# Kernel tuning notes

Hardware: AMD Instinct MI355X
Metric: run time of the kernel (lower is better)

Reference implementation:

```python
import jax, jax.numpy as jnp
import numpy as np

# --- PGA G(3,0,1) algebra tables, blade order matches gatr/ezgatr convention ---
_BLADES = [(), (0,), (1,), (2,), (3,), (0, 1), (0, 2), (0, 3), (1, 2), (1, 3), (2, 3),
           (0, 1, 2), (0, 1, 3), (0, 2, 3), (1, 2, 3), (0, 1, 2, 3)]
_IDX = {b: i for i, b in enumerate(_BLADES)}
_METRIC = (0, 1, 1, 1)  # e0^2 = 0, e1^2 = e2^2 = e3^2 = 1


def _mul_blades(a, b):
    elems = list(a) + list(b)
    sign = 1
    done = False
    while not done:
        done = True
        t = 0
        while t < len(elems) - 1:
            if elems[t] == elems[t + 1]:
                if _METRIC[elems[t]] == 0:
                    return 0, ()
                del elems[t + 1], elems[t]
                done = False
            elif elems[t] > elems[t + 1]:
                elems[t], elems[t + 1] = elems[t + 1], elems[t]
                sign = -sign
                done = False
                t += 1
            else:
                t += 1
    return sign, tuple(elems)


def _perm_sign(seq):
    inv = sum(1 for i in range(len(seq)) for j in range(i + 1, len(seq)) if seq[i] > seq[j])
    return -1 if inv % 2 else 1


def _build_tables():
    # geometric product Cayley table: x*y = einsum('ijk,i,j->k', GP, x, y)
    gp = np.zeros((16, 16, 16), np.float32)
    for i, a in enumerate(_BLADES):
        for j, b in enumerate(_BLADES):
            s, r = _mul_blades(a, b)
            if s:
                gp[i, j, _IDX[r]] = s
    # right-complement dual: dual(e_b) = dsign[b] * e_comp(b), with e_b ^ dual(e_b) = e0123
    comp = {b: tuple(e for e in range(4) if e not in b) for b in _BLADES}
    dsign = {b: _perm_sign(list(b) + list(comp[b])) for b in _BLADES}
    # join Cayley table: J(x, y) = undual(dual(x) ^ dual(y))
    jc = np.zeros((16, 16, 16), np.float32)
    for i, a in enumerate(_BLADES):
        for j, b in enumerate(_BLADES):
            da, db = comp[a], comp[b]
            if set(da) & set(db):
                continue
            w = _perm_sign(list(da) + list(db))  # wedge sign
            m = tuple(sorted(da + db))
            k = comp[m]  # undual(e_m) = dsign[k] * e_k since dual(e_k) = dsign[k] * e_m
            jc[i, j, _IDX[k]] = dsign[a] * dsign[b] * w * dsign[k]
    # EquiLinear basis: 5 grade projections + 4 maps 'left-multiply by e0'; [9, out16, in16]
    basis = np.zeros((9, 16, 16), np.float32)
    for idx, b in enumerate(_BLADES):
        basis[len(b), idx, idx] = 1.0
        if 0 not in b and len(b) < 4:
            basis[5 + len(b), _IDX[(0,) + b], idx] = 1.0  # e0 * e_b = +e_{0b}
    return gp, jc, basis


_GP, _JC, _BASIS = _build_tables()
GP = jnp.asarray(_GP)
JC = jnp.asarray(_JC)
BASIS = jnp.asarray(_BASIS)


def equi_linear(x, w, b):
    # x: [..., c_in, 16], w: [c_out, c_in, 9], b: [c_out] bias on scalar component
    out = jnp.einsum('oia,akj,...ij->...ok', w, BASIS, x)
    return out.at[..., 0].add(b)


def setup_inputs() -> dict:
    key = jax.random.key(0)
    ks = jax.random.split(key, 6)
    B, T, H, I = 8, 8192, 32, 32  # batch, context, hidden channels, intermediate channels
    x = jax.random.normal(ks[0], (B, T, H, 16), jnp.float32)
    ref = jax.random.normal(ks[1], (B, T, 1, 16), jnp.float32)
    w_bil = jax.random.normal(ks[2], (2 * I, H, 9), jnp.float32) / np.sqrt(9.0 * H)
    b_bil = jax.random.normal(ks[3], (2 * I,), jnp.float32) * 0.02
    w_out = jax.random.normal(ks[4], (H, I, 9), jnp.float32) / np.sqrt(9.0 * I)
    b_out = jax.random.normal(ks[5], (H,), jnp.float32) * 0.02
    return {"x": x, "ref": ref, "w_bil": w_bil, "b_bil": b_bil, "w_out": w_out, "b_out": b_out}


def reference(x, ref, w_bil, b_bil, w_out, b_out):
    h = equi_linear(x, w_bil, b_bil)  # [B, T, 2*I, 16]
    si = h.shape[-2] // 4             # size_channels_intermediate // 2
    lg, rg, lj, rj = (h[..., t * si:(t + 1) * si, :] for t in range(4))
    gp = jnp.einsum('ijk,...ci,...cj->...ck', GP, lg, rg)
    join = ref[..., 15:16] * jnp.einsum('ijk,...ci,...cj->...ck', JC, lj, rj)
    return equi_linear(jnp.concatenate([gp, join], axis=-2), w_out, b_out)
```

## Files before the change

kernel.cpp:

```cpp
#include <hip/hip_runtime.h>

typedef unsigned int uint_t;

constexpr int MASK_OF_IDX[16] = {0,1,2,4,8,3,5,9,6,10,12,7,11,13,14,15};
constexpr int IDX_OF_MASK[16] = {0,1,2,5,3,6,8,11,4,7,9,12,10,13,14,15};

constexpr int popc4(int v){ int c=0; for(int b=0;b<4;++b) c += (v>>b)&1; return c; }
constexpr int reorder_sign(int a,int b){ int s=0; for(int j=0;j<4;++j) if((b>>j)&1) s += popc4(a>>(j+1)); return (s&1)?-1:1; }
constexpr int dsign_mask(int m){ int comp=(~m)&15; int s=0; for(int j=0;j<4;++j) if((comp>>j)&1) s += popc4(m>>(j+1)); return (s&1)?-1:1; }

struct Tab { int n; int e[256]; };
constexpr Tab build_gp(){
  Tab t{}; t.n=0;
  for(int i=0;i<16;++i) for(int j=0;j<16;++j){
    int a=MASK_OF_IDX[i], b=MASK_OF_IDX[j];
    if(a&b&1) continue;
    int k=IDX_OF_MASK[a^b];
    int s=reorder_sign(a,b);
    t.e[t.n++] = i | (j<<4) | (k<<8) | ((s<0)?(1<<12):0);
  }
  return t;
}
constexpr Tab build_jc(){
  Tab t{}; t.n=0;
  for(int i=0;i<16;++i) for(int j=0;j<16;++j){
    int a=MASK_OF_IDX[i], b=MASK_OF_IDX[j];
    int da=(~a)&15, db=(~b)&15;
    if(da&db) continue;
    int m=da|db, km=(~m)&15;
    int k=IDX_OF_MASK[km];
    int s=reorder_sign(da,db)*dsign_mask(a)*dsign_mask(b)*dsign_mask(km);
    t.e[t.n++] = i | (j<<4) | (k<<8) | ((s<0)?(1<<12):0);
  }
  return t;
}
constexpr Tab GPT = build_gp();
constexpr Tab JCT = build_jc();
static_assert(GPT.n==192, "gp nnz");
static_assert(JCT.n==81,  "jc nnz");

__device__ __forceinline__ void eqstepv(float* acc, const float* xv, const float4* w4){
  float w[12];
  *reinterpret_cast<float4*>(w+0) = w4[0];
  *reinterpret_cast<float4*>(w+4) = w4[1];
  *reinterpret_cast<float4*>(w+8) = w4[2];
  constexpr int G[16] = {0,1,1,1,1,2,2,2,2,2,2,3,3,3,3,4};
#pragma unroll
  for (int k=0;k<16;++k) acc[k] += w[G[k]]*xv[k];
  acc[1]  += w[5]*xv[0];
  acc[5]  += w[6]*xv[2];
  acc[6]  += w[6]*xv[3];
  acc[7]  += w[6]*xv[4];
  acc[11] += w[7]*xv[8];
  acc[12] += w[7]*xv[9];
  acc[13] += w[7]*xv[10];
  acc[15] += w[8]*xv[14];
}

#define TT   64
#define NTHR 1024
#define WP1_FLOATS (32*16*48)
#define WP3_FLOATS (32*16*24)

__global__ void gatr_pack_w(const float* __restrict__ wbil,
                            const float* __restrict__ wout,
                            float* __restrict__ wp){
  int tid = blockIdx.x*blockDim.x + threadIdx.x;
  if (tid < WP1_FLOATS){
    int k = tid % 12, q = (tid/12)&3, c = (tid/48)&15, i = tid/768;
    wp[tid] = (k<9) ? wbil[(((q<<4)+c)*32 + i)*9 + k] : 0.f;
  } else if (tid < WP1_FLOATS + WP3_FLOATS){
    int u = tid - WP1_FLOATS;
    int k = u % 12, h = (u/12)&1, g = (u/24)&15, ci = u/384;
    wp[tid] = (k<9) ? wout[(((h<<4)+g)*32 + ci)*9 + k] : 0.f;
  }
}

__global__ __launch_bounds__(NTHR, 4) void gatr_fused_kernel(
    const float* __restrict__ xg, const float* __restrict__ refg,
    const float* __restrict__ wp, const float* __restrict__ bbilg,
    const float* __restrict__ boutg, float* __restrict__ outg)
{
  __shared__ float4 LB[TT * 128];

  const int tid = threadIdx.x;
  const size_t tok0 = (size_t)blockIdx.x * TT;
  const int t = tid & 63;
  const int c = __builtin_amdgcn_readfirstlane(tid >> 6);

  const float refv = refg[(tok0 + t)*16 + 15];

  {
    const float4* xg4 = reinterpret_cast<const float4*>(xg + tok0*512);
#pragma unroll
    for (int j=0;j<8;++j){
      int g = tid + j*NTHR;
      int tau = g >> 7, f4 = g & 127;
      LB[(tau<<7) + ((f4 + tau) & 127)] = xg4[g];
    }
  }
  __syncthreads();

  const int tbase = t << 7;

  float gp[16], jn[16];
  {
    float A0[16], A1[16], A2[16], A3[16];
#pragma unroll
    for (int k=0;k<16;++k){ A0[k]=0.f; A1[k]=0.f; A2[k]=0.f; A3[k]=0.f; }

    const float4* w4 = reinterpret_cast<const float4*>(wp) + c*12;
    for (int i=0;i<32;++i){
      float xv[16];
      const int o = (i<<2) + t;
      *reinterpret_cast<float4*>(xv+ 0) = LB[tbase + ( o      & 127)];
      *reinterpret_cast<float4*>(xv+ 4) = LB[tbase + ((o + 1) & 127)];
      *reinterpret_cast<float4*>(xv+ 8) = LB[tbase + ((o + 2) & 127)];
      *reinterpret_cast<float4*>(xv+12) = LB[tbase + ((o + 3) & 127)];
      eqstepv(A0, xv, w4 + 0);
      eqstepv(A1, xv, w4 + 3);
      eqstepv(A2, xv, w4 + 6);
      eqstepv(A3, xv, w4 + 9);
      w4 += 192;
    }
    A0[0] += bbilg[c];
    A1[0] += bbilg[c + 16];
    A2[0] += bbilg[c + 32];
    A3[0] += bbilg[c + 48];

#pragma unroll
    for (int k=0;k<16;++k){ gp[k]=0.f; jn[k]=0.f; }
#pragma unroll
    for (int e=0;e<192;++e){
      const int p = GPT.e[e];
      float v = A0[p & 15] * A1[(p >> 4) & 15];
      if (p & (1<<12)) gp[(p >> 8) & 15] -= v; else gp[(p >> 8) & 15] += v;
    }
#pragma unroll
    for (int e=0;e<81;++e){
      const int p = JCT.e[e];
      float v = A2[p & 15] * A3[(p >> 4) & 15];
      if (p & (1<<12)) jn[(p >> 8) & 15] -= v; else jn[(p >> 8) & 15] += v;
    }
#pragma unroll
    for (int k=0;k<16;++k) jn[k] *= refv;
  }
  __syncthreads();

  {
#pragma unroll
    for (int r=0;r<4;++r){
      LB[tbase + (((c     )*4 + r + t) & 127)] = make_float4(gp[4*r], gp[4*r+1], gp[4*r+2], gp[4*r+3]);
      LB[tbase + (((c + 16)*4 + r + t) & 127)] = make_float4(jn[4*r], jn[4*r+1], jn[4*r+2], jn[4*r+3]);
    }
  }
  __syncthreads();

  float B0a[16], B1a[16];
  {
#pragma unroll
    for (int k=0;k<16;++k){ B0a[k]=0.f; B1a[k]=0.f; }

    const float4* w6 = reinterpret_cast<const float4*>(wp + WP1_FLOATS) + c*6;
    for (int cin=0; cin<32; ++cin){
      float yv[16];
      const int o = (cin<<2) + t;
      *reinterpret_cast<float4*>(yv+ 0) = LB[tbase + ( o      & 127)];
      *reinterpret_cast<float4*>(yv+ 4) = LB[tbase + ((o + 1) & 127)];
      *reinterpret_cast<float4*>(yv+ 8) = LB[tbase + ((o + 2) & 127)];
      *reinterpret_cast<float4*>(yv+12) = LB[tbase + ((o + 3) & 127)];
      eqstepv(B0a, yv, w6 + 0);
      eqstepv(B1a, yv, w6 + 3);
      w6 += 96;
    }
    B0a[0] += boutg[c];
    B1a[0] += boutg[c + 16];
  }
  __syncthreads();

  {
#pragma unroll
    for (int r=0;r<4;++r){
      LB[tbase + (((c     )*4 + r + t) & 127)] = make_float4(B0a[4*r], B0a[4*r+1], B0a[4*r+2], B0a[4*r+3]);
      LB[tbase + (((c + 16)*4 + r + t) & 127)] = make_float4(B1a[4*r], B1a[4*r+1], B1a[4*r+2], B1a[4*r+3]);
    }
  }
  __syncthreads();
  {
    float4* og4 = reinterpret_cast<float4*>(outg + tok0*512);
#pragma unroll
    for (int j=0;j<8;++j){
      int g = tid + j*NTHR;
      int tau = g >> 7, f4 = g & 127;
      og4[g] = LB[(tau<<7) + ((f4 + tau) & 127)];
    }
  }
}

extern "C" void kernel_launch(void* const* d_in, const int* in_sizes, int n_in,
                              void* d_out, int out_size, void* d_ws, size_t ws_size,
                              hipStream_t stream) {
  const float* x    = (const float*)d_in[0];
  const float* ref  = (const float*)d_in[1];
  const float* wbil = (const float*)d_in[2];
  const float* bbil = (const float*)d_in[3];
  const float* wout = (const float*)d_in[4];
  const float* bout = (const float*)d_in[5];
  float* out = (float*)d_out;
  float* wp  = (float*)d_ws;

  hipLaunchKernelGGL(gatr_pack_w,
                     dim3((WP1_FLOATS + WP3_FLOATS + 255)/256), dim3(256), 0, stream,
                     wbil, wout, wp);

  const int ntok = in_sizes[0] / 512;
  const int grid = ntok / TT;
  hipLaunchKernelGGL(gatr_fused_kernel, dim3(grid), dim3(NTHR), 0, stream,
                     x, ref, wp, bbil, bout, out);
}
```

Measured before the change: 427.9 us.

## Halve LDS tile by staging channels in two passes and store output directly

The shared buffer shrinks from 128 to 64 float4 per token. The input is loaded in two halves of 16 channels, and the gp and join results are staged one after the other through the same smaller buffer, so more blocks can fit per CU (launch bounds raised to 8). The final transposed write-out through LDS is replaced by direct per-thread float4 stores of each output row. This adds extra barriers and leaves the global stores uncoalesced, since each thread writes 64 bytes at a 2KB token stride. The tighter register budget from the higher occupancy target also risks spills.

New measurement: 1.645 ms. 285% more time.

```diff
diff --git a/kernel.cpp b/kernel.cpp
--- a/kernel.cpp
+++ b/kernel.cpp
@@ -38,6 +38,14 @@
 constexpr Tab JCT = build_jc();
 static_assert(GPT.n==192, "gp nnz");
 static_assert(JCT.n==81,  "jc nnz");
+
+__device__ __forceinline__ void st16(float* p, const float* v){
+  float4* q = (float4*)p;
+  q[0] = make_float4(v[0],v[1],v[2],v[3]);
+  q[1] = make_float4(v[4],v[5],v[6],v[7]);
+  q[2] = make_float4(v[8],v[9],v[10],v[11]);
+  q[3] = make_float4(v[12],v[13],v[14],v[15]);
+}
 
 __device__ __forceinline__ void eqstepv(float* acc, const float* xv, const float4* w4){
   float w[12];
@@ -76,12 +84,12 @@
   }
 }
 
-__global__ __launch_bounds__(NTHR, 4) void gatr_fused_kernel(
+__global__ __launch_bounds__(NTHR, 8) void gatr_fused_kernel(
     const float* __restrict__ xg, const float* __restrict__ refg,
     const float* __restrict__ wp, const float* __restrict__ bbilg,
     const float* __restrict__ boutg, float* __restrict__ outg)
 {
-  __shared__ float4 LB[TT * 128];
+  __shared__ float4 LB[TT * 64];
 
   const int tid = threadIdx.x;
   const size_t tok0 = (size_t)blockIdx.x * TT;
@@ -90,111 +98,112 @@
 
   const float refv = refg[(tok0 + t)*16 + 15];
 
-  {
-    const float4* xg4 = reinterpret_cast<const float4*>(xg + tok0*512);
-#pragma unroll
-    for (int j=0;j<8;++j){
+  const int tbase = t << 6;
+
+  float A0[16], A1[16], A2[16], A3[16];
+#pragma unroll
+  for (int k=0;k<16;++k){ A0[k]=0.f; A1[k]=0.f; A2[k]=0.f; A3[k]=0.f; }
+
+  const float4* w4 = reinterpret_cast<const float4*>(wp) + c*12;
+  const float4* xg4 = reinterpret_cast<const float4*>(xg + tok0*512);
+
+  for (int h=0; h<2; ++h){
+#pragma unroll
+    for (int j=0;j<4;++j){
       int g = tid + j*NTHR;
-      int tau = g >> 7, f4 = g & 127;
-      LB[(tau<<7) + ((f4 + tau) & 127)] = xg4[g];
+      int tau = g >> 6, s = g & 63;
+      LB[(tau<<6) + ((s + tau) & 63)] = xg4[tau*128 + h*64 + s];
     }
-  }
-  __syncthreads();
-
-  const int tbase = t << 7;
-
-  float gp[16], jn[16];
-  {
-    float A0[16], A1[16], A2[16], A3[16];
-#pragma unroll
-    for (int k=0;k<16;++k){ A0[k]=0.f; A1[k]=0.f; A2[k]=0.f; A3[k]=0.f; }
-
-    const float4* w4 = reinterpret_cast<const float4*>(wp) + c*12;
-    for (int i=0;i<32;++i){
+    __syncthreads();
+
+    for (int ii=0; ii<16; ++ii){
       float xv[16];
-      const int o = (i<<2) + t;
-      *reinterpret_cast<float4*>(xv+ 0) = LB[tbase + ( o      & 127)];
-      *reinterpret_cast<float4*>(xv+ 4) = LB[tbase + ((o + 1) & 127)];
-      *reinterpret_cast<float4*>(xv+ 8) = LB[tbase + ((o + 2) & 127)];
-      *reinterpret_cast<float4*>(xv+12) = LB[tbase + ((o + 3) & 127)];
+      const int o = (ii<<2) + t;
+      *reinterpret_cast<float4*>(xv+ 0) = LB[tbase + ( o      & 63)];
+      *reinterpret_cast<float4*>(xv+ 4) = LB[tbase + ((o + 1) & 63)];
+      *reinterpret_cast<float4*>(xv+ 8) = LB[tbase + ((o + 2) & 63)];
+      *reinterpret_cast<float4*>(xv+12) = LB[tbase + ((o + 3) & 63)];
       eqstepv(A0, xv, w4 + 0);
       eqstepv(A1, xv, w4 + 3);
       eqstepv(A2, xv, w4 + 6);
       eqstepv(A3, xv, w4 + 9);
       w4 += 192;
     }
-    A0[0] += bbilg[c];
-    A1[0] += bbilg[c + 16];
-    A2[0] += bbilg[c + 32];
-    A3[0] += bbilg[c + 48];
-
-#pragma unroll
-    for (int k=0;k<16;++k){ gp[k]=0.f; jn[k]=0.f; }
-#pragma unroll
-    for (int e=0;e<192;++e){
-      const int p = GPT.e[e];
-      float v = A0[p & 15] * A1[(p >> 4) & 15];
-      if (p & (1<<12)) gp[(p >> 8) & 15] -= v; else gp[(p >> 8) & 15] += v;
-    }
-#pragma unroll
-    for (int e=0;e<81;++e){
-      const int p = JCT.e[e];
-      float v = A2[p & 15] * A3[(p >> 4) & 15];
-      if (p & (1<<12)) jn[(p >> 8) & 15] -= v; else jn[(p >> 8) & 15] += v;
-    }
-#pragma unroll
-    for (int k=0;k<16;++k) jn[k] *= refv;
-  }
+    __syncthreads();
+  }
+
+  A0[0] += bbilg[c];
+  A1[0] += bbilg[c + 16];
+  A2[0] += bbilg[c + 32];
+  A3[0] += bbilg[c + 48];
+
+  float gp[16];
+#pragma unroll
+  for (int k=0;k<16;++k) gp[k]=0.f;
+#pragma unroll
+  for (int e=0;e<192;++e){
+    const int p = GPT.e[e];
+    float v = A0[p & 15] * A1[(p >> 4) & 15];
+    if (p & (1<<12)) gp[(p >> 8) & 15] -= v; else gp[(p >> 8) & 15] += v;
+  }
+#pragma unroll
+  for (int r=0;r<4;++r)
+    LB[tbase + (((c<<2) + r + t) & 63)] = make_float4(gp[4*r], gp[4*r+1], gp[4*r+2], gp[4*r+3]);
+
+  float jn[16];
+#pragma unroll
+  for (int k=0;k<16;++k) jn[k]=0.f;
+#pragma unroll
+  for (int e=0;e<81;++e){
+    const int p = JCT.e[e];
+    float v = A2[p & 15] * A3[(p >> 4) & 15];
+    if (p & (1<<12)) jn[(p >> 8) & 15] -= v; else jn[(p >> 8) & 15] += v;
+  }
+#pragma unroll
+  for (int k=0;k<16;++k) jn[k] *= refv;
+
   __syncthreads();
 
-  {
-#pragma unroll
-    for (int r=0;r<4;++r){
-      LB[tbase + (((c     )*4 + r + t) & 127)] = make_float4(gp[4*r], gp[4*r+1], gp[4*r+2], gp[4*r+3]);
-      LB[tbase + (((c + 16)*4 + r + t) & 127)] = make_float4(jn[4*r], jn[4*r+1], jn[4*r+2], jn[4*r+3]);
-    }
+  float B0a[16], B1a[16];
+#pragma unroll
+  for (int k=0;k<16;++k){ B0a[k]=0.f; B1a[k]=0.f; }
+
+  const float4* w6 = reinterpret_cast<const float4*>(wp + WP1_FLOATS) + c*6;
+  for (int cin=0; cin<16; ++cin){
+    float yv[16];
+    const int o = (cin<<2) + t;
+    *reinterpret_cast<float4*>(yv+ 0) = LB[tbase + ( o      & 63)];
+    *reinterpret_cast<float4*>(yv+ 4) = LB[tbase + ((o + 1) & 63)];
+    *reinterpret_cast<float4*>(yv+ 8) = LB[tbase + ((o + 2) & 63)];
+    *reinterpret_cast<float4*>(yv+12) = LB[tbase + ((o + 3) & 63)];
+    eqstepv(B0a, yv, w6 + 0);
+    eqstepv(B1a, yv, w6 + 3);
+    w6 += 96;
   }
   __syncthreads();
 
-  float B0a[16], B1a[16];
-  {
-#pragma unroll
-    for (int k=0;k<16;++k){ B0a[k]=0.f; B1a[k]=0.f; }
-
-    const float4* w6 = reinterpret_cast<const float4*>(wp + WP1_FLOATS) + c*6;
-    for (int cin=0; cin<32; ++cin){
-      float yv[16];
-      const int o = (cin<<2) + t;
-      *reinterpret_cast<float4*>(yv+ 0) = LB[tbase + ( o      & 127)];
-      *reinterpret_cast<float4*>(yv+ 4) = LB[tbase + ((o + 1) & 127)];
-      *reinterpret_cast<float4*>(yv+ 8) = LB[tbase + ((o + 2) & 127)];
-      *reinterpret_cast<float4*>(yv+12) = LB[tbase + ((o + 3) & 127)];
-      eqstepv(B0a, yv, w6 + 0);
-      eqstepv(B1a, yv, w6 + 3);
-      w6 += 96;
-    }
-    B0a[0] += boutg[c];
-    B1a[0] += boutg[c + 16];
-  }
+#pragma unroll
+  for (int r=0;r<4;++r)
+    LB[tbase + (((c<<2) + r + t) & 63)] = make_float4(jn[4*r], jn[4*r+1], jn[4*r+2], jn[4*r+3]);
   __syncthreads();
 
-  {
-#pragma unroll
-    for (int r=0;r<4;++r){
-      LB[tbase + (((c     )*4 + r + t) & 127)] = make_float4(B0a[4*r], B0a[4*r+1], B0a[4*r+2], B0a[4*r+3]);
-      LB[tbase + (((c + 16)*4 + r + t) & 127)] = make_float4(B1a[4*r], B1a[4*r+1], B1a[4*r+2], B1a[4*r+3]);
-    }
-  }
-  __syncthreads();
-  {
-    float4* og4 = reinterpret_cast<float4*>(outg + tok0*512);
-#pragma unroll
-    for (int j=0;j<8;++j){
-      int g = tid + j*NTHR;
-      int tau = g >> 7, f4 = g & 127;
-      og4[g] = LB[(tau<<7) + ((f4 + tau) & 127)];
-    }
-  }
+  for (int cin=0; cin<16; ++cin){
+    float yv[16];
+    const int o = (cin<<2) + t;
+    *reinterpret_cast<float4*>(yv+ 0) = LB[tbase + ( o      & 63)];
+    *reinterpret_cast<float4*>(yv+ 4) = LB[tbase + ((o + 1) & 63)];
+    *reinterpret_cast<float4*>(yv+ 8) = LB[tbase + ((o + 2) & 63)];
+    *reinterpret_cast<float4*>(yv+12) = LB[tbase + ((o + 3) & 63)];
+    eqstepv(B0a, yv, w6 + 0);
+    eqstepv(B1a, yv, w6 + 3);
+    w6 += 96;
+  }
+  B0a[0] += boutg[c];
+  B1a[0] += boutg[c + 16];
+
+  float* orow = outg + (tok0 + t)*512;
+  st16(orow + (c     )*16, B0a);
+  st16(orow + (c + 16)*16, B1a);
 }
 
 extern "C" void kernel_launch(void* const* d_in, const int* in_sizes, int n_in,
```

## Split fused GATr kernel into two kernels with global intermediate buffer

Applied to the files above, without the earlier changes.

Splits the single fused kernel into two: the first computes the bilinear layer and the geometric/join products and writes the intermediate to a channel-major global workspace, and the second reads it back and applies the output equi-linear layer. This removes two block-wide barriers and the shared-memory round trips between stages, and each kernel may get lower register pressure. In exchange it adds a full write and read of a 128 MB intermediate through global memory plus an extra launch. The old fused kernel is kept as a fallback when the workspace is too small.

Result: slower. 478.0 us (+11.7%).

```diff
diff --git a/kernel.cpp b/kernel.cpp
--- a/kernel.cpp
+++ b/kernel.cpp
@@ -39,6 +39,14 @@
 static_assert(GPT.n==192, "gp nnz");
 static_assert(JCT.n==81,  "jc nnz");
 
+__device__ __forceinline__ void st16(float* p, const float* v){
+  float4* q = (float4*)p;
+  q[0] = make_float4(v[0],v[1],v[2],v[3]);
+  q[1] = make_float4(v[4],v[5],v[6],v[7]);
+  q[2] = make_float4(v[8],v[9],v[10],v[11]);
+  q[3] = make_float4(v[12],v[13],v[14],v[15]);
+}
+
 __device__ __forceinline__ void eqstepv(float* acc, const float* xv, const float4* w4){
   float w[12];
   *reinterpret_cast<float4*>(w+0) = w4[0];
@@ -61,6 +69,7 @@
 #define NTHR 1024
 #define WP1_FLOATS (32*16*48)
 #define WP3_FLOATS (32*16*24)
+#define WP_FLOATS  (WP1_FLOATS + WP3_FLOATS)
 
 __global__ void gatr_pack_w(const float* __restrict__ wbil,
                             const float* __restrict__ wout,
@@ -74,6 +83,134 @@
     int k = u % 12, h = (u/12)&1, g = (u/24)&15, ci = u/384;
     wp[tid] = (k<9) ? wout[(((h<<4)+g)*32 + ci)*9 + k] : 0.f;
   }
+}
+
+
+__global__ __launch_bounds__(NTHR, 4) void gatr_p12(
+    const float* __restrict__ xg, const float* __restrict__ refg,
+    const float* __restrict__ wp, const float* __restrict__ bbilg,
+    float4* __restrict__ yt, int ntok)
+{
+  __shared__ float4 LB[TT * 128];
+
+  const int tid = threadIdx.x;
+  const size_t tok0 = (size_t)blockIdx.x * TT;
+  const int t = tid & 63;
+  const int c = __builtin_amdgcn_readfirstlane(tid >> 6);
+
+  const float refv = refg[(tok0 + t)*16 + 15];
+
+  {
+    const float4* xg4 = reinterpret_cast<const float4*>(xg + tok0*512);
+#pragma unroll
+    for (int j=0;j<8;++j){
+      int g = tid + j*NTHR;
+      int tau = g >> 7, f4 = g & 127;
+      LB[(tau<<7) + ((f4 + tau) & 127)] = xg4[g];
+    }
+  }
+  __syncthreads();
+
+  const int tbase = t << 7;
+
+  float A0[16], A1[16], A2[16], A3[16];
+#pragma unroll
+  for (int k=0;k<16;++k){ A0[k]=0.f; A1[k]=0.f; A2[k]=0.f; A3[k]=0.f; }
+
+  const float4* w4 = reinterpret_cast<const float4*>(wp) + c*12;
+  for (int i=0;i<32;++i){
+    float xv[16];
+    const int o = (i<<2) + t;
+    *reinterpret_cast<float4*>(xv+ 0) = LB[tbase + ( o      & 127)];
+    *reinterpret_cast<float4*>(xv+ 4) = LB[tbase + ((o + 1) & 127)];
+    *reinterpret_cast<float4*>(xv+ 8) = LB[tbase + ((o + 2) & 127)];
+    *reinterpret_cast<float4*>(xv+12) = LB[tbase + ((o + 3) & 127)];
+    eqstepv(A0, xv, w4 + 0);
+    eqstepv(A1, xv, w4 + 3);
+    eqstepv(A2, xv, w4 + 6);
+    eqstepv(A3, xv, w4 + 9);
+    w4 += 192;
+  }
+  A0[0] += bbilg[c];
+  A1[0] += bbilg[c + 16];
+  A2[0] += bbilg[c + 32];
+  A3[0] += bbilg[c + 48];
+
+  float gp[16];
+#pragma unroll
+  for (int k=0;k<16;++k) gp[k]=0.f;
+#pragma unroll
+  for (int e=0;e<192;++e){
+    const int p = GPT.e[e];
+    float v = A0[p & 15] * A1[(p >> 4) & 15];
+    if (p & (1<<12)) gp[(p >> 8) & 15] -= v; else gp[(p >> 8) & 15] += v;
+  }
+#pragma unroll
+  for (int r=0;r<4;++r)
+    yt[(size_t)((c<<2) + r)*ntok + tok0 + t] =
+        make_float4(gp[4*r], gp[4*r+1], gp[4*r+2], gp[4*r+3]);
+
+  float jn[16];
+#pragma unroll
+  for (int k=0;k<16;++k) jn[k]=0.f;
+#pragma unroll
+  for (int e=0;e<81;++e){
+    const int p = JCT.e[e];
+    float v = A2[p & 15] * A3[(p >> 4) & 15];
+    if (p & (1<<12)) jn[(p >> 8) & 15] -= v; else jn[(p >> 8) & 15] += v;
+  }
+#pragma unroll
+  for (int r=0;r<4;++r){
+    float4 o4 = make_float4(jn[4*r]*refv, jn[4*r+1]*refv, jn[4*r+2]*refv, jn[4*r+3]*refv);
+    yt[(size_t)(((c+16)<<2) + r)*ntok + tok0 + t] = o4;
+  }
+}
+
+__global__ __launch_bounds__(NTHR, 4) void gatr_p3(
+    const float4* __restrict__ yt, const float* __restrict__ wp,
+    const float* __restrict__ boutg, float* __restrict__ outg, int ntok)
+{
+  __shared__ float4 LB[TT * 128];
+
+  const int tid = threadIdx.x;
+  const size_t tok0 = (size_t)blockIdx.x * TT;
+  const int t = tid & 63;
+  const int c = __builtin_amdgcn_readfirstlane(tid >> 6);
+
+  {
+#pragma unroll
+    for (int j=0;j<8;++j){
+      int g = tid + j*NTHR;
+      int row = g >> 6, s = g & 63;
+      LB[(s<<7) + ((row + s) & 127)] = yt[(size_t)row*ntok + tok0 + s];
+    }
+  }
+  __syncthreads();
+
+  const int tbase = t << 7;
+
+  float B0a[16], B1a[16];
+#pragma unroll
+  for (int k=0;k<16;++k){ B0a[k]=0.f; B1a[k]=0.f; }
+
+  const float4* w6 = reinterpret_cast<const float4*>(wp + WP1_FLOATS) + c*6;
+  for (int cin=0; cin<32; ++cin){
+    float yv[16];
+    const int o = (cin<<2) + t;
+    *reinterpret_cast<float4*>(yv+ 0) = LB[tbase + ( o      & 127)];
+    *reinterpret_cast<float4*>(yv+ 4) = LB[tbase + ((o + 1) & 127)];
+    *reinterpret_cast<float4*>(yv+ 8) = LB[tbase + ((o + 2) & 127)];
+    *reinterpret_cast<float4*>(yv+12) = LB[tbase + ((o + 3) & 127)];
+    eqstepv(B0a, yv, w6 + 0);
+    eqstepv(B1a, yv, w6 + 3);
+    w6 += 96;
+  }
+  B0a[0] += boutg[c];
+  B1a[0] += boutg[c + 16];
+
+  float* orow = outg + (tok0 + t)*512;
+  st16(orow + (c     )*16, B0a);
+  st16(orow + (c + 16)*16, B1a);
 }
 
 __global__ __launch_bounds__(NTHR, 4) void gatr_fused_kernel(
@@ -209,12 +346,24 @@
   float* out = (float*)d_out;
   float* wp  = (float*)d_ws;
 
-  hipLaunchKernelGGL(gatr_pack_w,
-                     dim3((WP1_FLOATS + WP3_FLOATS + 255)/256), dim3(256), 0, stream,
-                     wbil, wout, wp);
-
   const int ntok = in_sizes[0] / 512;
   const int grid = ntok / TT;
-  hipLaunchKernelGGL(gatr_fused_kernel, dim3(grid), dim3(NTHR), 0, stream,
-                     x, ref, wp, bbil, bout, out);
-}
+
+  hipLaunchKernelGGL(gatr_pack_w,
+                     dim3((WP_FLOATS + 255)/256), dim3(256), 0, stream,
+                     wbil, wout, wp);
+
+  const size_t ybytes = (size_t)ntok * 2048;
+  const size_t need   = (size_t)WP_FLOATS*4 + ybytes;
+
+  if (ws_size >= need) {
+    float4* yt = reinterpret_cast<float4*>((char*)d_ws + (size_t)WP_FLOATS*4);
+    hipLaunchKernelGGL(gatr_p12, dim3(grid), dim3(NTHR), 0, stream,
+                       x, ref, wp, bbil, yt, ntok);
+    hipLaunchKernelGGL(gatr_p3, dim3(grid), dim3(NTHR), 0, stream,
+                       yt, wp, bout, out, ntok);
+  } else {
+    hipLaunchKernelGGL(gatr_fused_kernel, dim3(grid), dim3(NTHR), 0, stream,
+                       x, ref, wp, bbil, bout, out);
+  }
+}
```
